# Kernel optimization log

Measured on AMD Instinct MI355X. Metric: run time of the kernel, lower is better.

Reference implementation:

```python
import jax, jax.numpy as jnp
import numpy as np

B, T, D, H, R = 8, 2048, 1024, 1024, 128
R_MAX, R_MIN, MAX_PHASE = 1.0, 0.0, 6.28


def setup_inputs() -> dict:
    key = jax.random.key(0)
    ks = jax.random.split(key, 10)
    x = jax.random.normal(ks[0], (B, T, D), dtype=jnp.float32)
    # nu_log / theta_log init as in the torch module constructor
    u1 = jax.random.uniform(ks[1], (H,), dtype=jnp.float32)
    inner = u1 * (R_MAX ** 2 - R_MIN ** 2) + R_MIN ** 2
    nu_log = jnp.log(-0.5 * jnp.log(inner + 1e-6) + 1e-6)
    u2 = jax.random.uniform(ks[2], (H,), dtype=jnp.float32)
    theta_log = jnp.log(MAX_PHASE * u2 + 1e-6)
    U1 = jax.random.normal(ks[3], (D, R), dtype=jnp.float32) / np.sqrt(D)
    U2 = jax.random.normal(ks[4], (D, R), dtype=jnp.float32) / np.sqrt(D)
    V1 = jax.random.normal(ks[5], (R, H), dtype=jnp.float32) / np.sqrt(R)
    V2 = jax.random.normal(ks[6], (R, H), dtype=jnp.float32) / np.sqrt(R)
    hc1_init = jax.random.normal(ks[7], (B, H), dtype=jnp.float32) * 0.1
    hc2_init = jax.random.normal(ks[8], (B, H), dtype=jnp.float32) * 0.1
    return {"x": x, "nu_log": nu_log, "theta_log": theta_log,
            "U1": U1, "U2": U2, "V1": V1, "V2": V2,
            "hc1_init": hc1_init, "hc2_init": hc2_init}


def _combine(left, right):
    # Compose complex rotations g+i*phi and accumulate rotated biases:
    # A = A_r * A_l ; b = A_r * b_l + b_r  (complex arithmetic in real pairs)
    gL, pL, bxL, byL = left
    gR, pR, bxR, byR = right
    g_new = gR * gL - pR * pL
    p_new = pR * gL + gR * pL
    bx_new = gR * bxL - pR * byL + bxR
    by_new = pR * bxL + gR * byL + byR
    return (g_new, p_new, bx_new, by_new)


def reference(x, nu_log, theta_log, U1, U2, V1, V2, hc1_init, hc2_init):
    r = jnp.exp(-jnp.exp(nu_log))                      # [H]
    theta = jnp.exp(theta_log)                         # [H]
    g = r * jnp.cos(theta)
    phi = r * jnp.sin(theta)
    gamma = jnp.sqrt(jnp.clip(1.0 - r * r, 0.0))
    # Low-rank input projections: [B,T,D] -> [B,T,R] -> [B,T,H]
    u1 = jnp.einsum('btr,rh->bth', jnp.einsum('btd,dr->btr', x, U1), V1)
    u2 = jnp.einsum('btr,rh->bth', jnp.einsum('btd,dr->btr', x, U2), V2)
    bx = u1 * gamma                                    # [B,T,H]
    by = u2 * gamma
    Bb, Tt, Hh = bx.shape
    gT = jnp.broadcast_to(g, (Bb, Tt, Hh))
    pT = jnp.broadcast_to(phi, (Bb, Tt, Hh))
    # Inclusive parallel scan over time (Hillis-Steele equivalent)
    gA, pA, Bx, By = jax.lax.associative_scan(_combine, (gT, pT, bx, by), axis=1)
    # c_t = A_t * c_0 + B_t  (complex mul in real pairs)
    c0x = hc1_init[:, None, :]
    c0y = hc2_init[:, None, :]
    c1 = gA * c0x - pA * c0y + Bx                      # [B,T,H]
    c2 = pA * c0x + gA * c0y + By
    # activation = identity (default nn.Identity in the module)
    y = jnp.concatenate([c1, c2], axis=-1)             # [B,T,2H]
    return y, c1[:, -1, :], c2[:, -1, :]
```

## Files before the change

kernel.cpp:

```cpp
#include <hip/hip_runtime.h>


using u16 = unsigned short;
using frag_ab = __attribute__((ext_vector_type(8))) short;
using frag_cd = __attribute__((ext_vector_type(4))) float;

__device__ __forceinline__ u16 f2bf(float f) {
    union { float f; unsigned u; } v; v.f = f;
    unsigned r = v.u + 0x7FFFu + ((v.u >> 16) & 1u);
    return (u16)(r >> 16);
}
__device__ __forceinline__ float bf2f(u16 s) {
    union { unsigned u; float f; } v; v.u = ((unsigned)s) << 16;
    return v.f;
}
__device__ __forceinline__ frag_cd mfma16(frag_ab a, frag_ab b, frag_cd c) {
    return __builtin_amdgcn_mfma_f32_16x16x32_bf16(a, b, c, 0, 0, 0);
}
__device__ __forceinline__ void lambda_of(const float* nu_log, const float* theta_log,
                                          int h, float& g, float& ph, float& gam)
{
    float rr = expf(-expf(nu_log[h]));
    float th = expf(theta_log[h]);
    g = rr * cosf(th);
    ph = rr * sinf(th);
    gam = sqrtf(fmaxf(1.0f - rr * rr, 0.0f));
}

__global__ __launch_bounds__(256) void k0_pack(
    const float* __restrict__ U1, const float* __restrict__ U2,
    const float* __restrict__ V1, const float* __restrict__ V2,
    u16* __restrict__ Ubfp, u16* __restrict__ Vt)
{
    int idx = blockIdx.x * 256 + threadIdx.x;
    if (idx < 32768) {
        int kg = idx & 127, n = idx >> 7;
        const float* Us = (n < 128) ? U1 : U2;
        int col = n & 127;
        u16 tmp[8];
#pragma unroll
        for (int j = 0; j < 8; ++j)
            tmp[j] = f2bf(Us[(size_t)(kg * 8 + j) * 128 + col]);
        *(uint4*)&Ubfp[((size_t)(kg >> 3) * 256 + n) * 64 + (kg & 7) * 8] = *(uint4*)tmp;
    } else {
        int i2 = idx - 32768;
        int kg = i2 & 15, h = (i2 >> 4) & 1023, br = i2 >> 14;
        const float* Vs = br ? V2 : V1;
        u16 tmp[8];
#pragma unroll
        for (int j = 0; j < 8; ++j)
            tmp[j] = f2bf(Vs[(size_t)(kg * 8 + j) * 1024 + h]);
        *(uint4*)&Vt[((size_t)br * 1024 + h) * 128 + (kg ^ (h & 15)) * 8] = *(uint4*)tmp;
    }
}

__global__ __launch_bounds__(256, 2) void kB_fused(
    const float* __restrict__ x, const u16* __restrict__ Ubfp, const u16* __restrict__ Vt,
    const float* __restrict__ nu_log, const float* __restrict__ theta_log,
    float2* __restrict__ agg, u16* __restrict__ u_ws)
{
    __shared__ __align__(16) u16 smem[24576];
    const int tid = threadIdx.x;
    const int t0 = blockIdx.x * 32;
    const int wave = tid >> 6, lane = tid & 63;
    const int lm = lane & 15, q = lane >> 4;
    char* smb = (char*)smem;

    const int rowA = tid >> 3, kcA = tid & 7;
    frag_cd acc1[2][4] = {};
    const float* xsrc = x + (size_t)(t0 + rowA) * 1024 + kcA * 8;
    const char* bsrc = (const char*)Ubfp;

    float4 pA0 = *(const float4*)xsrc;
    float4 pA1 = *(const float4*)(xsrc + 4);

    for (int kt = 0; kt < 16; ++kt) {
        {
            u16 ap[8] = { f2bf(pA0.x), f2bf(pA0.y), f2bf(pA0.z), f2bf(pA0.w),
                          f2bf(pA1.x), f2bf(pA1.y), f2bf(pA1.z), f2bf(pA1.w) };
            *(uint4*)&smem[16640 + (rowA >> 3) * 520 + (rowA & 7) * 64 + kcA * 8] = *(uint4*)ap;
        }
#pragma unroll
        for (int i = 0; i < 8; ++i) {
            int blk = wave * 8 + i;
            __builtin_amdgcn_global_load_lds(
                (const __attribute__((address_space(1))) void*)(bsrc + (size_t)kt * 32768 + blk * 1024 + lane * 16),
                (__attribute__((address_space(3))) void*)(smb + blk * 1040), 16, 0, 0);
        }
        __syncthreads();
        if (kt + 1 < 16) {
            pA0 = *(const float4*)(xsrc + (kt + 1) * 64);
            pA1 = *(const float4*)(xsrc + (kt + 1) * 64 + 4);
        }
        frag_ab a[2], b[4];
#pragma unroll
        for (int ksub = 0; ksub < 2; ++ksub) {
#pragma unroll
            for (int m2 = 0; m2 < 2; ++m2) {
                int ra = m2 * 16 + lm;
                a[m2] = *(const frag_ab*)&smem[16640 + (ra >> 3) * 520 + (ra & 7) * 64 + ksub * 32 + q * 8];
            }
#pragma unroll
            for (int n4 = 0; n4 < 4; ++n4) {
                int nb = wave * 64 + n4 * 16 + lm;
                b[n4] = *(const frag_ab*)&smem[(nb >> 3) * 520 + (nb & 7) * 64 + ksub * 32 + q * 8];
            }
#pragma unroll
            for (int m2 = 0; m2 < 2; ++m2)
#pragma unroll
                for (int n4 = 0; n4 < 4; ++n4)
                    acc1[m2][n4] = mfma16(a[m2], b[n4], acc1[m2][n4]);
        }
        __syncthreads();
    }
#pragma unroll
    for (int m2 = 0; m2 < 2; ++m2)
#pragma unroll
        for (int n4 = 0; n4 < 4; ++n4)
#pragma unroll
            for (int i = 0; i < 4; ++i) {
                int t = m2 * 16 + q * 4 + i;
                int col = wave * 64 + n4 * 16 + lm;
                int gcol = col >> 3;
                int swz = (gcol & 16) | ((gcol ^ t) & 15);
                smem[t * 256 + swz * 8 + (col & 7)] = f2bf(acc1[m2][n4][i]);
            }
    __syncthreads();

    const int hl = tid & 127, sc = tid >> 7;
    const int b = t0 >> 11;
    const int ncb = (t0 & 2047) >> 4;

    for (int c = 0; c < 8; ++c) {
        frag_cd acc2[2][2][2] = {};
#pragma unroll
        for (int br = 0; br < 2; ++br) {
            const char* vsrc = (const char*)Vt + ((size_t)br * 1024 + c * 128) * 256;
#pragma unroll
            for (int i = 0; i < 8; ++i) {
                int blk = wave * 8 + i;
                __builtin_amdgcn_global_load_lds(
                    (const __attribute__((address_space(1))) void*)(vsrc + blk * 1024 + lane * 16),
                    (__attribute__((address_space(3))) void*)(smb + 16384 + blk * 1024 + lane * 16), 16, 0, 0);
            }
            __syncthreads();
#pragma unroll
            for (int ks = 0; ks < 4; ++ks) {
                int gk = br * 16 + ks * 4 + q;
                int ra0 = lm, ra1 = 16 + lm;
                frag_ab a0 = *(const frag_ab*)&smem[ra0 * 256 + ((gk & 16) | ((gk ^ ra0) & 15)) * 8];
                frag_ab a1 = *(const frag_ab*)&smem[ra1 * 256 + ((gk & 16) | ((gk ^ ra1) & 15)) * 8];
                int gv = ks * 4 + q;
                int nb0 = wave * 32 + lm, nb1 = nb0 + 16;
                frag_ab b0 = *(const frag_ab*)&smem[8192 + nb0 * 128 + ((gv ^ (nb0 & 15)) * 8)];
                frag_ab b1 = *(const frag_ab*)&smem[8192 + nb1 * 128 + ((gv ^ (nb1 & 15)) * 8)];
                acc2[br][0][0] = mfma16(a0, b0, acc2[br][0][0]);
                acc2[br][0][1] = mfma16(a0, b1, acc2[br][0][1]);
                acc2[br][1][0] = mfma16(a1, b0, acc2[br][1][0]);
                acc2[br][1][1] = mfma16(a1, b1, acc2[br][1][1]);
            }
            __syncthreads();
        }
#pragma unroll
        for (int br = 0; br < 2; ++br)
#pragma unroll
            for (int m2 = 0; m2 < 2; ++m2)
#pragma unroll
                for (int n2 = 0; n2 < 2; ++n2)
#pragma unroll
                    for (int i = 0; i < 4; ++i) {
                        int t = m2 * 16 + q * 4 + i;
                        int hloc = wave * 32 + n2 * 16 + lm;
                        int sw = ((hloc >> 3) ^ (t & 15)) * 8 + (hloc & 7);
                        smem[8192 + br * 4096 + t * 128 + sw] = f2bf(acc2[br][m2][n2][i]);
                    }
        __syncthreads();
        {
            int h = c * 128 + hl;
            float g, ph, gam;
            lambda_of(nu_log, theta_log, h, g, ph, gam);
            float bx = 0.f, by = 0.f;
#pragma unroll
            for (int j = 0; j < 16; ++j) {
                int tt = sc * 16 + j;
                int sw = ((hl >> 3) ^ (tt & 15)) * 8 + (hl & 7);
                float u1 = bf2f(smem[8192 + tt * 128 + sw]);
                float u2 = bf2f(smem[8192 + 4096 + tt * 128 + sw]);
                float ex = gam * u1, ey = gam * u2;
                float nx = fmaf(g, bx, fmaf(-ph, by, ex));
                float ny = fmaf(ph, bx, fmaf(g, by, ey));
                bx = nx; by = ny;
            }
            agg[((size_t)b * 128 + ncb + sc) * 1024 + h] = make_float2(bx, by);
        }
        {
            size_t ub = ((size_t)blockIdx.x * 8 + c) * 8192;
#pragma unroll
            for (int i = 0; i < 4; ++i) {
                uint4 v = *(const uint4*)&smem[(size_t)8192 + (i * 256 + tid) * 8];
                *(uint4*)&u_ws[ub + (size_t)(i * 256 + tid) * 8] = v;
            }
        }
        __syncthreads();
    }
}

__global__ __launch_bounds__(64) void k3_scan(
    float2* __restrict__ agg_carry, const float* __restrict__ nu_log,
    const float* __restrict__ theta_log, const float* __restrict__ hc1,
    const float* __restrict__ hc2)
{
    const int idx = blockIdx.x * 64 + threadIdx.x;
    const int b = idx >> 10, h = idx & 1023;
    float g, ph, gam;
    lambda_of(nu_log, theta_log, h, g, ph, gam);
    float ax = g, ay = ph;
#pragma unroll
    for (int i = 0; i < 4; ++i) { float nx = ax * ax - ay * ay, ny = 2.f * ax * ay; ax = nx; ay = ny; }
    float cx = hc1[idx], cy = hc2[idx];
    float2* acp = agg_carry + (size_t)b * 128 * 1024 + h;
#pragma unroll 8
    for (int c = 0; c < 128; ++c) {
        float2 a = acp[(size_t)c * 1024];
        acp[(size_t)c * 1024] = make_float2(cx, cy);
        float nx = fmaf(ax, cx, fmaf(-ay, cy, a.x));
        float ny = fmaf(ay, cx, fmaf(ax, cy, a.y));
        cx = nx; cy = ny;
    }
}

__global__ __launch_bounds__(256) void k4_apply(
    const u16* __restrict__ u_ws,
    const float* __restrict__ nu_log, const float* __restrict__ theta_log,
    const float2* __restrict__ carries, float* __restrict__ out)
{
    const int tid = threadIdx.x;
    const int c = blockIdx.x;
    const int t0 = blockIdx.y * 128;
    const int hg = tid & 31, ck = tid >> 5;
    const int h = c * 128 + hg * 4;
    const int b = t0 >> 11;
    const int tloc = t0 & 2047;
    const int nc = (tloc >> 4) + ck;

    float g[4], ph[4], gam[4];
#pragma unroll
    for (int k = 0; k < 4; ++k) lambda_of(nu_log, theta_log, h + k, g[k], ph[k], gam[k]);

    const float2* cp = carries + ((size_t)b * 128 + nc) * 1024 + h;
    float4 cab = *(const float4*)cp;
    float4 ccd = *(const float4*)(cp + 2);
    float cx[4] = { cab.x, cab.z, ccd.x, ccd.z };
    float cy[4] = { cab.y, cab.w, ccd.y, ccd.w };

    const int tb32 = (t0 >> 5) + (ck >> 1);
    const u16* ut = u_ws + ((size_t)tb32 * 8 + c) * 8192;
    const int gi = hg >> 1, off = (hg & 1) * 4;
    float* yb = out + (size_t)b * (2048 * 2048);

#pragma unroll
    for (int j = 0; j < 16; ++j) {
        int tt = (ck & 1) * 16 + j;
        int sw = ((gi ^ (tt & 15)) * 8) + off;
        uint2 r1 = *(const uint2*)&ut[tt * 128 + sw];
        uint2 r2 = *(const uint2*)&ut[4096 + tt * 128 + sw];
        u16 a1[4]; *(uint2*)a1 = r1;
        u16 a2[4]; *(uint2*)a2 = r2;
#pragma unroll
        for (int k = 0; k < 4; ++k) {
            float u1 = bf2f(a1[k]), u2 = bf2f(a2[k]);
            float ex = gam[k] * u1, ey = gam[k] * u2;
            float nx = fmaf(g[k], cx[k], fmaf(-ph[k], cy[k], ex));
            float ny = fmaf(ph[k], cx[k], fmaf(g[k], cy[k], ey));
            cx[k] = nx; cy[k] = ny;
        }
        int t = tloc + ck * 16 + j;
        *(float4*)&yb[(size_t)t * 2048 + h]        = make_float4(cx[0], cx[1], cx[2], cx[3]);
        *(float4*)&yb[(size_t)t * 2048 + 1024 + h] = make_float4(cy[0], cy[1], cy[2], cy[3]);
    }
    if (tloc + ck * 16 == 2032) {
        *(float4*)&out[(size_t)33554432 + (size_t)b * 1024 + h] =
            make_float4(cx[0], cx[1], cx[2], cx[3]);
        *(float4*)&out[(size_t)33554432 + 8192 + (size_t)b * 1024 + h] =
            make_float4(cy[0], cy[1], cy[2], cy[3]);
    }
}

extern "C" void kernel_launch(void* const* d_in, const int* in_sizes, int n_in,
                              void* d_out, int out_size, void* d_ws, size_t ws_size,
                              hipStream_t stream) {
    const float* x         = (const float*)d_in[0];
    const float* nu_log    = (const float*)d_in[1];
    const float* theta_log = (const float*)d_in[2];
    const float* U1        = (const float*)d_in[3];
    const float* U2        = (const float*)d_in[4];
    const float* V1        = (const float*)d_in[5];
    const float* V2        = (const float*)d_in[6];
    const float* hc1       = (const float*)d_in[7];
    const float* hc2       = (const float*)d_in[8];

    float2* agg  = (float2*)((char*)d_ws + (size_t)8 * 1024 * 1024);
    u16*    Vt   = (u16*)((char*)d_ws + (size_t)16 * 1024 * 1024);
    u16*    Ubfp = (u16*)((char*)d_ws + (size_t)16 * 1024 * 1024 + 512 * 1024);
    u16*    u_ws = (u16*)((char*)d_ws + (size_t)17 * 1024 * 1024);

    k0_pack<<<256, 256, 0, stream>>>(U1, U2, V1, V2, Ubfp, Vt);
    kB_fused<<<512, 256, 0, stream>>>(x, Ubfp, Vt, nu_log, theta_log, agg, u_ws);
    k3_scan<<<128, 64, 0, stream>>>(agg, nu_log, theta_log, hc1, hc2);
    k4_apply<<<dim3(8, 128), 256, 0, stream>>>(u_ws, nu_log, theta_log, agg, (float*)d_out);
}
```

Measured before the change: 271.6 us.

## Fuse carry scan into apply kernel by recomputing prefix carries per thread

Removes the separate serial carry-scan kernel. Each apply thread now folds the chunk aggregates from the start of the sequence up to its own chunk, starting from the initial state. This eliminates one kernel launch and the low-occupancy sequential pass. In exchange it adds quadratic redundant loads and FMAs over chunks, with a long dependent loop of up to 127 steps in the apply kernel.

After: 286.2 us. +5.4%, slower.

```diff
diff --git a/kernel.cpp b/kernel.cpp
--- a/kernel.cpp
+++ b/kernel.cpp
@@ -205,34 +205,11 @@
     }
 }
 
-__global__ __launch_bounds__(64) void k3_scan(
-    float2* __restrict__ agg_carry, const float* __restrict__ nu_log,
-    const float* __restrict__ theta_log, const float* __restrict__ hc1,
-    const float* __restrict__ hc2)
-{
-    const int idx = blockIdx.x * 64 + threadIdx.x;
-    const int b = idx >> 10, h = idx & 1023;
-    float g, ph, gam;
-    lambda_of(nu_log, theta_log, h, g, ph, gam);
-    float ax = g, ay = ph;
-#pragma unroll
-    for (int i = 0; i < 4; ++i) { float nx = ax * ax - ay * ay, ny = 2.f * ax * ay; ax = nx; ay = ny; }
-    float cx = hc1[idx], cy = hc2[idx];
-    float2* acp = agg_carry + (size_t)b * 128 * 1024 + h;
-#pragma unroll 8
-    for (int c = 0; c < 128; ++c) {
-        float2 a = acp[(size_t)c * 1024];
-        acp[(size_t)c * 1024] = make_float2(cx, cy);
-        float nx = fmaf(ax, cx, fmaf(-ay, cy, a.x));
-        float ny = fmaf(ay, cx, fmaf(ax, cy, a.y));
-        cx = nx; cy = ny;
-    }
-}
-
 __global__ __launch_bounds__(256) void k4_apply(
     const u16* __restrict__ u_ws,
     const float* __restrict__ nu_log, const float* __restrict__ theta_log,
-    const float2* __restrict__ carries, float* __restrict__ out)
+    const float2* __restrict__ agg, const float* __restrict__ hc1,
+    const float* __restrict__ hc2, float* __restrict__ out)
 {
     const int tid = threadIdx.x;
     const int c = blockIdx.x;
@@ -247,11 +224,34 @@
 #pragma unroll
     for (int k = 0; k < 4; ++k) lambda_of(nu_log, theta_log, h + k, g[k], ph[k], gam[k]);
 
-    const float2* cp = carries + ((size_t)b * 128 + nc) * 1024 + h;
-    float4 cab = *(const float4*)cp;
-    float4 ccd = *(const float4*)(cp + 2);
-    float cx[4] = { cab.x, cab.z, ccd.x, ccd.z };
-    float cy[4] = { cab.y, cab.w, ccd.y, ccd.w };
+    float ax[4], ay[4];
+#pragma unroll
+    for (int k = 0; k < 4; ++k) {
+        float axx = g[k], ayy = ph[k];
+#pragma unroll
+        for (int i = 0; i < 4; ++i) { float nx = axx * axx - ayy * ayy, ny = 2.f * axx * ayy; axx = nx; ayy = ny; }
+        ax[k] = axx; ay[k] = ayy;
+    }
+    float4 h1 = *(const float4*)&hc1[(size_t)b * 1024 + h];
+    float4 h2 = *(const float4*)&hc2[(size_t)b * 1024 + h];
+    float cx[4] = { h1.x, h1.y, h1.z, h1.w };
+    float cy[4] = { h2.x, h2.y, h2.z, h2.w };
+    {
+        const float2* ap = agg + (size_t)b * 128 * 1024 + h;
+        for (int j = 0; j < nc; ++j) {
+            float4 a01 = *(const float4*)ap;
+            float4 a23 = *(const float4*)(ap + 2);
+            float axv[4] = { a01.x, a01.z, a23.x, a23.z };
+            float ayv[4] = { a01.y, a01.w, a23.y, a23.w };
+#pragma unroll
+            for (int k = 0; k < 4; ++k) {
+                float nx = fmaf(ax[k], cx[k], fmaf(-ay[k], cy[k], axv[k]));
+                float ny = fmaf(ay[k], cx[k], fmaf(ax[k], cy[k], ayv[k]));
+                cx[k] = nx; cy[k] = ny;
+            }
+            ap += 1024;
+        }
+    }
 
     const int tb32 = (t0 >> 5) + (ck >> 1);
     const u16* ut = u_ws + ((size_t)tb32 * 8 + c) * 8192;
@@ -306,6 +306,6 @@
 
     k0_pack<<<256, 256, 0, stream>>>(U1, U2, V1, V2, Ubfp, Vt);
     kB_fused<<<512, 256, 0, stream>>>(x, Ubfp, Vt, nu_log, theta_log, agg, u_ws);
-    k3_scan<<<128, 64, 0, stream>>>(agg, nu_log, theta_log, hc1, hc2);
-    k4_apply<<<dim3(8, 128), 256, 0, stream>>>(u_ws, nu_log, theta_log, agg, (float*)d_out);
-}
+    k4_apply<<<dim3(8, 128), 256, 0, stream>>>(u_ws, nu_log, theta_log, agg, hc1, hc2,
+                                               (float*)d_out);
+}
```
